# Performance work log

Measured on AMD Instinct MI355X. Metric: run time of the kernel, lower is better.

## Reference

```python
import jax, jax.numpy as jnp
import numpy as np

D_MODEL = 1024
NUM_HEADS = 16
D_K = D_MODEL // NUM_HEADS
B, S = 4, 2048


def setup_inputs() -> dict:
    key = jax.random.key(0)
    ks = jax.random.split(key, 12)
    scale = 1.0 / np.sqrt(D_MODEL)
    inp = {
        "Q": jax.random.normal(ks[0], (B, S, D_MODEL), dtype=jnp.float32),
        "K": jax.random.normal(ks[1], (B, S, D_MODEL), dtype=jnp.float32),
        "V": jax.random.normal(ks[2], (B, S, D_MODEL), dtype=jnp.float32),
        # causal mask broadcast over batch and heads; masked_fill where mask==0
        "mask": jnp.tril(jnp.ones((S, S), dtype=jnp.int32))[None, None, :, :],
        "Wq": jax.random.normal(ks[3], (D_MODEL, D_MODEL), dtype=jnp.float32) * scale,
        "bq": jnp.zeros((D_MODEL,), dtype=jnp.float32),
        "Wk": jax.random.normal(ks[4], (D_MODEL, D_MODEL), dtype=jnp.float32) * scale,
        "bk": jnp.zeros((D_MODEL,), dtype=jnp.float32),
        "Wv": jax.random.normal(ks[5], (D_MODEL, D_MODEL), dtype=jnp.float32) * scale,
        "bv": jnp.zeros((D_MODEL,), dtype=jnp.float32),
        "Wo": jax.random.normal(ks[6], (D_MODEL, D_MODEL), dtype=jnp.float32) * scale,
        "bo": jnp.zeros((D_MODEL,), dtype=jnp.float32),
    }
    return inp


def _split_heads(x):
    b, s, _ = x.shape
    return x.reshape(b, s, NUM_HEADS, D_K).transpose(0, 2, 1, 3)  # [B,H,S,Dk]


def reference(Q, K, V, mask, Wq, bq, Wk, bk, Wv, bv, Wo, bo):
    # torch nn.Linear: x @ W.T + b
    q = _split_heads(Q @ Wq.T + bq)
    k = _split_heads(K @ Wk.T + bk)
    v = _split_heads(V @ Wv.T + bv)
    scores = jnp.einsum("bhsd,bhtd->bhst", q, k) / jnp.sqrt(jnp.float32(D_K))
    scores = jnp.where(mask == 0, jnp.float32(-1e9), scores)
    probs = jax.nn.softmax(scores, axis=-1)  # dropout is identity in eval mode
    ctx = jnp.einsum("bhst,bhtd->bhsd", probs, v)
    ctx = ctx.transpose(0, 2, 1, 3).reshape(Q.shape[0], Q.shape[1], D_MODEL)
    out = ctx @ Wo.T + bo
    return out, probs
```

## Files before the change

kernel.cpp:

```cpp
#include <hip/hip_runtime.h>
#include <stdint.h>

typedef unsigned short u16;
typedef unsigned int u32;
typedef __attribute__((ext_vector_type(2))) unsigned int u32x2;
typedef __attribute__((ext_vector_type(8))) short short8;
typedef __attribute__((ext_vector_type(4))) float f32x4;
typedef __attribute__((ext_vector_type(4))) unsigned int u32x4;

#define SEQ 2048
#define DM 1024
#define NH 16
#define NBH 64
#define MR 8192

#define GLOAD16(g, l) __builtin_amdgcn_global_load_lds( \
    (const __attribute__((address_space(1))) void*)(g), \
    (__attribute__((address_space(3))) void*)(l), 16, 0, 0)

#define VMCNT(N) asm volatile("s_waitcnt vmcnt(" #N ")" ::: "memory")

__device__ __forceinline__ u16 f2bf(float f) {
  u32 u = __float_as_uint(f);
  u32 r = u + 0x7fffu + ((u >> 16) & 1u);
  return (u16)(r >> 16);
}
__device__ __forceinline__ u32 cvtpk_bf16(float lo, float hi) {
  u32 r;
  asm("v_cvt_pk_bf16_f32 %0, %1, %2" : "=v"(r) : "v"(lo), "v"(hi));
  return r;
}

__global__ __launch_bounds__(256) void cvt_all(
    const float* __restrict__ Q, const float* __restrict__ K, const float* __restrict__ V,
    const float* __restrict__ Wq, const float* __restrict__ Wk, const float* __restrict__ Wv,
    const float* __restrict__ Wo,
    u16* __restrict__ dQ, u16* __restrict__ dK, u16* __restrict__ dV,
    u16* __restrict__ dWq, u16* __restrict__ dWk, u16* __restrict__ dWv, u16* __restrict__ dWo) {
  int b = blockIdx.x;
  const float* s; u16* d; size_t off;
  if (b < 4096)       { s = Q;  d = dQ;  off = (size_t)b * 2048; }
  else if (b < 8192)  { s = K;  d = dK;  off = (size_t)(b - 4096) * 2048; }
  else if (b < 12288) { s = V;  d = dV;  off = (size_t)(b - 8192) * 2048; }
  else if (b < 12800) { s = Wq; d = dWq; off = (size_t)(b - 12288) * 2048; }
  else if (b < 13312) { s = Wk; d = dWk; off = (size_t)(b - 12800) * 2048; }
  else if (b < 13824) { s = Wv; d = dWv; off = (size_t)(b - 13312) * 2048; }
  else                { s = Wo; d = dWo; off = (size_t)(b - 13824) * 2048; }
  size_t i = off + (size_t)threadIdx.x * 8;
  float4 x = *(const float4*)(s + i);
  float4 y = *(const float4*)(s + i + 4);
  u32x4 o;
  o.x = (u32)f2bf(x.x) | ((u32)f2bf(x.y) << 16);
  o.y = (u32)f2bf(x.z) | ((u32)f2bf(x.w) << 16);
  o.z = (u32)f2bf(y.x) | ((u32)f2bf(y.y) << 16);
  o.w = (u32)f2bf(y.z) | ((u32)f2bf(y.w) << 16);
  *(u32x4*)(d + i) = o;
}

__device__ __forceinline__ void gemm_body(
    const u16* __restrict__ A, const u16* __restrict__ Bw, const float* __restrict__ bias,
    void* __restrict__ Cp, int wg, int MODE) {
  const int bn = wg & 7;
  const int bm = wg >> 3;
  __shared__ u16 As[2][128 * 64];
  __shared__ u16 Bs[2][128 * 64];
  const int tid = threadIdx.x;
  const int lane = tid & 63, wave = tid >> 6;
  const int wr = wave >> 1, wc = wave & 1;
  const int g16 = lane >> 4, l16 = lane & 15;
  f32x4 acc[4][4] = {};

  const int srow = lane >> 3;
  const int sblk = (lane & 7) ^ srow;
  const u16* Abase = A + (size_t)(bm * 128) * DM + sblk * 8;
  const u16* Bbase = Bw + (size_t)(bn * 128) * DM + sblk * 8;

  auto stage = [&](int kt) {
#pragma unroll
    for (int i = 0; i < 4; ++i) {
      const int r0 = wave * 32 + i * 8;
      GLOAD16(Abase + (size_t)(r0 + srow) * DM + kt * 64, (char*)As[kt & 1] + r0 * 128);
      GLOAD16(Bbase + (size_t)(r0 + srow) * DM + kt * 64, (char*)Bs[kt & 1] + r0 * 128);
    }
  };

  stage(0);
  for (int kt = 0; kt < 16; ++kt) {
    VMCNT(0);
    __builtin_amdgcn_s_barrier();
    if (kt + 1 < 16) stage(kt + 1);
    const char* Ab = (const char*)As[kt & 1];
    const char* Bb = (const char*)Bs[kt & 1];
#pragma unroll
    for (int ks = 0; ks < 2; ++ks) {
      short8 af[4], bfr[4];
#pragma unroll
      for (int m = 0; m < 4; ++m) {
        const int r = wr * 64 + m * 16 + l16;
        af[m] = *(const short8*)(Ab + ((r * 128 + ks * 64 + g16 * 16) ^ ((r & 7) << 4)));
      }
#pragma unroll
      for (int n = 0; n < 4; ++n) {
        const int r = wc * 64 + n * 16 + l16;
        bfr[n] = *(const short8*)(Bb + ((r * 128 + ks * 64 + g16 * 16) ^ ((r & 7) << 4)));
      }
#pragma unroll
      for (int m = 0; m < 4; ++m)
#pragma unroll
        for (int n = 0; n < 4; ++n)
          acc[m][n] = __builtin_amdgcn_mfma_f32_16x16x32_bf16(af[m], bfr[n], acc[m][n], 0, 0, 0);
    }
  }
#pragma unroll
  for (int m = 0; m < 4; ++m)
#pragma unroll
    for (int n = 0; n < 4; ++n) {
      int col = bn * 128 + wc * 64 + n * 16 + l16;
      float bs = bias[col];
      if (MODE == 2) {
        int row0 = bm * 128 + wr * 64 + m * 16 + g16 * 4;
        int bb = row0 >> 11, ss = row0 & 2047;
        int hh = col >> 6, dd = col & 63;
        u32 lo = (u32)f2bf(acc[m][n][0] + bs) | ((u32)f2bf(acc[m][n][1] + bs) << 16);
        u32 hi = (u32)f2bf(acc[m][n][2] + bs) | ((u32)f2bf(acc[m][n][3] + bs) << 16);
        *(u32x2*)((u16*)Cp + (((size_t)(bb * NH + hh) * 64 + dd) * SEQ + ss)) = (u32x2){lo, hi};
      } else {
#pragma unroll
        for (int r = 0; r < 4; ++r) {
          int row = bm * 128 + wr * 64 + m * 16 + g16 * 4 + r;
          float v = acc[m][n][r] + bs;
          if (MODE == 0) {
            int bb = row >> 11, ss = row & 2047, hh = col >> 6, dd = col & 63;
            ((u16*)Cp)[((((size_t)bb * NH + hh) * SEQ + ss) << 6) + dd] = f2bf(v);
          } else {
            ((float*)Cp)[(size_t)row * DM + col] = v;
          }
        }
      }
    }
}

__global__ __launch_bounds__(256) void gemm_qkv(
    const u16* __restrict__ Qb, const u16* __restrict__ Wqb, const float* __restrict__ bq, u16* __restrict__ qhp,
    const u16* __restrict__ Kb, const u16* __restrict__ Wkb, const float* __restrict__ bk, u16* __restrict__ khp,
    const u16* __restrict__ Vb, const u16* __restrict__ Wvb, const float* __restrict__ bv, u16* __restrict__ vtp) {
  const int bid = blockIdx.x;
  const int sel = bid >> 9;
  const int inner = bid & 511;
  const int wg = (inner & 7) * 64 + (inner >> 3);
  if (sel == 0)      gemm_body(Qb, Wqb, bq, qhp, wg, 0);
  else if (sel == 1) gemm_body(Kb, Wkb, bk, khp, wg, 0);
  else               gemm_body(Vb, Wvb, bv, vtp, wg, 2);
}

__global__ __launch_bounds__(256) void gemm_out(
    const u16* __restrict__ A, const u16* __restrict__ Bw, const float* __restrict__ bias,
    float* __restrict__ Cp) {
  const int bid = blockIdx.x;
  const int wg = (bid & 7) * 64 + (bid >> 3);
  gemm_body(A, Bw, bias, Cp, wg, 1);
}

__global__ __launch_bounds__(512, 4) void attn_fwd(
    const u16* __restrict__ qh, const u16* __restrict__ kh, const u16* __restrict__ vt,
    float* __restrict__ probs, u16* __restrict__ ctx) {
  const int bid = blockIdx.x;
  const int wg = (bid & 7) * 128 + (bid >> 3);
  const int qt = 15 - (wg & 15);
  const int bh = wg >> 4;
  const int tid = threadIdx.x;
  const int lane = tid & 63, wave = tid >> 6;
  const int g16 = lane >> 4, l16 = lane & 15;
  __shared__ __align__(16) char SLDS[65536];
  char* Ps = SLDS + 49152;

  const int qglob = qt * 128 + wave * 16 + l16;
  short8 qf0, qf1;
  {
    const u16* qp = qh + ((size_t)bh * SEQ + qglob) * 64 + g16 * 8;
    qf0 = *(const short8*)qp;
    qf1 = *(const short8*)(qp + 32);
  }
  float lrow = 0.f;
  const float SL2 = 0.125f * 1.44269504088896f;

  const int srow = wave * 8 + (lane >> 3);
  const int sblk = (lane & 7) ^ (lane >> 3);
  const u16* kS = kh + ((size_t)bh * SEQ + srow) * 64 + sblk * 8;
  const u16* vS = vt + ((size_t)bh * 64 + srow) * SEQ + sblk * 8;

  auto qk64 = [&](const char* Kb, int ss, f32x4 (&sc)[4]) {
#pragma unroll
    for (int ks = 0; ks < 2; ++ks) {
      const short8 qf = ks ? qf1 : qf0;
#pragma unroll
      for (int f = 0; f < 4; ++f) {
        const int t = ss * 64 + f * 16 + l16;
        const short8 kb = *(const short8*)(Kb + ((t * 128 + ks * 64 + g16 * 16) ^ ((t & 7) << 4)));
        sc[f] = __builtin_amdgcn_mfma_f32_16x16x32_bf16(kb, qf, sc[f], 0, 0, 0);
      }
    }
  };

  const int nkA = qt + 1;
  auto stageA = [&](int kt) {
#pragma unroll
    for (int i = 0; i < 2; ++i)
      GLOAD16(kS + ((size_t)kt * 128 + i * 64) * 64,
              SLDS + (kt & 3) * 16384 + i * 8192 + wave * 1024);
  };
  stageA(0);
  if (nkA > 1) stageA(1);
  for (int kt = 0; kt < nkA; ++kt) {
    if (kt + 2 < nkA) { stageA(kt + 2); VMCNT(4); }
    else if (kt + 1 < nkA) VMCNT(2);
    else VMCNT(0);
    __builtin_amdgcn_s_barrier();
    const char* Kb = SLDS + (kt & 3) * 16384;
    float s = 0.f;
#pragma unroll
    for (int ss = 0; ss < 2; ++ss) {
      f32x4 sc[4] = {};
      __builtin_amdgcn_s_setprio(1);
      qk64(Kb, ss, sc);
      __builtin_amdgcn_s_setprio(0);
      const bool fullt = (kt * 128 + ss * 64 + 63 <= qt * 128 + wave * 16);
      if (fullt) {
#pragma unroll
        for (int f = 0; f < 4; ++f)
#pragma unroll
          for (int r = 0; r < 4; ++r)
            s += exp2f(sc[f][r] * SL2);
      } else {
#pragma unroll
        for (int f = 0; f < 4; ++f)
#pragma unroll
          for (int r = 0; r < 4; ++r) {
            const int k = kt * 128 + ss * 64 + f * 16 + g16 * 4 + r;
            s += (k <= qglob) ? exp2f(sc[f][r] * SL2) : 0.f;
          }
      }
    }
    s += __shfl_xor(s, 16);
    s += __shfl_xor(s, 32);
    lrow += s;
  }
  const float rinv = 1.f / lrow;

  f32x4 acc[4] = {};
  const size_t prowB = ((size_t)bh * SEQ + qglob) * SEQ;
  const int prow = wave * 16 + l16;
  const int nkt = 2 * qt + 2;

  __syncthreads();
  auto stageBK = [&](int kt) {
    GLOAD16(kS + (size_t)kt * 4096, SLDS + (kt % 3) * 8192 + wave * 1024);
  };
  auto stageBV = [&](int kt) {
    GLOAD16(vS + (size_t)kt * 64, SLDS + 24576 + (kt % 3) * 8192 + wave * 1024);
  };
  stageBK(0); stageBV(0);
  for (int kt = 0; kt < nkt; ++kt) {
    if (kt + 1 < nkt) {
      stageBK(kt + 1); stageBV(kt + 1);
      if (kt == 0) VMCNT(2); else VMCNT(6);
    } else {
      if (kt == 0) VMCNT(0); else VMCNT(4);
    }
    __builtin_amdgcn_s_barrier();
    const char* Kb = SLDS + (kt % 3) * 8192;
    const char* Vb = SLDS + 24576 + (kt % 3) * 8192;
    f32x4 sc[4] = {};
    __builtin_amdgcn_s_setprio(1);
    qk64(Kb, 0, sc);
    __builtin_amdgcn_s_setprio(0);
    const bool fullt = (kt * 64 + 63 <= qt * 128 + wave * 16);
#pragma unroll
    for (int f = 0; f < 4; ++f) {
      float pv[4];
      if (fullt) {
#pragma unroll
        for (int r = 0; r < 4; ++r) pv[r] = exp2f(sc[f][r] * SL2) * rinv;
      } else {
#pragma unroll
        for (int r = 0; r < 4; ++r) {
          const int k = kt * 64 + f * 16 + g16 * 4 + r;
          pv[r] = (k <= qglob) ? exp2f(sc[f][r] * SL2) * rinv : 0.f;
        }
      }
      *(f32x4*)(probs + prowB + kt * 64 + f * 16 + g16 * 4) =
          (f32x4){pv[0], pv[1], pv[2], pv[3]};
      u32x2 pk = {cvtpk_bf16(pv[0], pv[1]), cvtpk_bf16(pv[2], pv[3])};
      *(u32x2*)(Ps + ((prow * 128 + f * 32 + g16 * 8) ^ ((prow & 7) << 4))) = pk;
    }
    __builtin_amdgcn_s_setprio(1);
#pragma unroll
    for (int ks = 0; ks < 2; ++ks) {
      const short8 pa = *(const short8*)(Ps + ((prow * 128 + ks * 64 + g16 * 16) ^ ((prow & 7) << 4)));
#pragma unroll
      for (int cf = 0; cf < 4; ++cf) {
        const int dd = cf * 16 + l16;
        const short8 vb = *(const short8*)(Vb + ((dd * 128 + ks * 64 + g16 * 16) ^ ((dd & 7) << 4)));
        acc[cf] = __builtin_amdgcn_mfma_f32_16x16x32_bf16(pa, vb, acc[cf], 0, 0, 0);
      }
    }
    __builtin_amdgcn_s_setprio(0);
  }

  {
    const size_t zrow = ((size_t)bh * SEQ + qt * 128 + wave * 16 + (lane >> 2)) * SEQ;
    const int pcol = (lane & 3) * 16;
    const f32x4 z = {0.f, 0.f, 0.f, 0.f};
    for (int c0 = nkt * 64 + pcol; c0 < SEQ; c0 += 64) {
      float* dst = probs + zrow + c0;
      *(f32x4*)(dst) = z;
      *(f32x4*)(dst + 4) = z;
      *(f32x4*)(dst + 8) = z;
      *(f32x4*)(dst + 12) = z;
    }
  }

#pragma unroll
  for (int cf = 0; cf < 4; ++cf)
#pragma unroll
    for (int r = 0; r < 4; ++r) {
      const int srw = qt * 128 + wave * 16 + g16 * 4 + r;
      const size_t o = ((size_t)(bh >> 4) * SEQ + srw) * DM + (bh & 15) * 64 + cf * 16 + l16;
      ctx[o] = f2bf(acc[cf][r]);
    }
}

extern "C" void kernel_launch(void* const* d_in, const int* in_sizes, int n_in,
                              void* d_out, int out_size, void* d_ws, size_t ws_size,
                              hipStream_t stream) {
  (void)in_sizes; (void)n_in; (void)out_size; (void)ws_size;
  const float* Q  = (const float*)d_in[0];
  const float* K  = (const float*)d_in[1];
  const float* V  = (const float*)d_in[2];
  const float* Wq = (const float*)d_in[4];
  const float* bq = (const float*)d_in[5];
  const float* Wk = (const float*)d_in[6];
  const float* bk = (const float*)d_in[7];
  const float* Wv = (const float*)d_in[8];
  const float* bv = (const float*)d_in[9];
  const float* Wo = (const float*)d_in[10];
  const float* bo = (const float*)d_in[11];

  char* ws = (char*)d_ws;
  const size_t MB = 1024 * 1024;
  u16* Qb  = (u16*)(ws + 0 * MB);
  u16* Kb  = (u16*)(ws + 16 * MB);
  u16* Vb  = (u16*)(ws + 32 * MB);
  u16* Wqb = (u16*)(ws + 48 * MB);
  u16* Wkb = (u16*)(ws + 50 * MB);
  u16* Wvb = (u16*)(ws + 52 * MB);
  u16* Wob = (u16*)(ws + 54 * MB);
  u16* qhp = (u16*)(ws + 56 * MB);
  u16* khp = (u16*)(ws + 72 * MB);
  u16* vtp = (u16*)(ws + 88 * MB);
  u16* ctx = Kb;

  float* outp = (float*)d_out;
  float* probs = outp + (size_t)MR * DM;

  cvt_all<<<14336, 256, 0, stream>>>(Q, K, V, Wq, Wk, Wv, Wo, Qb, Kb, Vb, Wqb, Wkb, Wvb, Wob);
  gemm_qkv<<<1536, 256, 0, stream>>>(Qb, Wqb, bq, qhp, Kb, Wkb, bk, khp, Vb, Wvb, bv, vtp);
  attn_fwd<<<1024, 512, 0, stream>>>(qhp, khp, vtp, probs, ctx);
  gemm_out<<<512, 256, 0, stream>>>(ctx, Wob, bo, outp);
}
```

Baseline: 472.0 us.

## Enlarge attention K/V staging tiles and switch to double-buffered barrier-first pipeline

Pass A now stages 256 keys per iteration in two 32KB buffers instead of 128 keys in a four-deep ring. Pass B moves from 64-key to 128-key K/V tiles with a new swizzled V layout, double-buffered, issuing the next prefetch after the barrier. The goal is fewer barriers and loop iterations per tile, at the cost of raising LDS from 64KB to 80KB per block. That can lower occupancy under launch_bounds(512,4), and waiting on vmcnt(0) in pass A exposes more load latency.

```diff
diff --git a/kernel.cpp b/kernel.cpp
--- a/kernel.cpp
+++ b/kernel.cpp
@@ -171,8 +171,8 @@
   const int tid = threadIdx.x;
   const int lane = tid & 63, wave = tid >> 6;
   const int g16 = lane >> 4, l16 = lane & 15;
-  __shared__ __align__(16) char SLDS[65536];
-  char* Ps = SLDS + 49152;
+  __shared__ __align__(16) char SLDS[81920];
+  char* Ps = SLDS + 65536;
 
   const int qglob = qt * 128 + wave * 16 + l16;
   short8 qf0, qf1;
@@ -187,7 +187,10 @@
   const int srow = wave * 8 + (lane >> 3);
   const int sblk = (lane & 7) ^ (lane >> 3);
   const u16* kS = kh + ((size_t)bh * SEQ + srow) * 64 + sblk * 8;
-  const u16* vS = vt + ((size_t)bh * 64 + srow) * SEQ + sblk * 8;
+  const int vrow0 = wave * 8 + (lane >> 4);
+  const u16* vS0 = vt + ((size_t)bh * 64 + vrow0) * SEQ + (((lane & 15) ^ (vrow0 & 7)) * 8);
+  const int vrow1 = vrow0 + 4;
+  const u16* vS1 = vt + ((size_t)bh * 64 + vrow1) * SEQ + (((lane & 15) ^ (vrow1 & 7)) * 8);
 
   auto qk64 = [&](const char* Kb, int ss, f32x4 (&sc)[4]) {
 #pragma unroll
@@ -202,116 +205,121 @@
     }
   };
 
-  const int nkA = qt + 1;
+  const int ntokA = (qt + 1) * 128;
+  const int n256 = (qt + 2) >> 1;
   auto stageA = [&](int kt) {
+#pragma unroll
+    for (int i = 0; i < 4; ++i)
+      GLOAD16(kS + ((size_t)kt * 256 + i * 64) * 64,
+              SLDS + (kt & 1) * 32768 + i * 8192 + wave * 1024);
+  };
+  stageA(0);
+  for (int kt = 0; kt < n256; ++kt) {
+    VMCNT(0);
+    __builtin_amdgcn_s_barrier();
+    if (kt + 1 < n256) stageA(kt + 1);
+    const char* Kb = SLDS + (kt & 1) * 32768;
+    float s = 0.f;
+#pragma unroll
+    for (int ss = 0; ss < 4; ++ss) {
+      const int t0 = kt * 256 + ss * 64;
+      if (t0 >= ntokA) break;
+      f32x4 sc[4] = {};
+      __builtin_amdgcn_s_setprio(1);
+      qk64(Kb, ss, sc);
+      __builtin_amdgcn_s_setprio(0);
+      const bool fullt = (t0 + 63 <= qt * 128 + wave * 16);
+      if (fullt) {
+#pragma unroll
+        for (int f = 0; f < 4; ++f)
+#pragma unroll
+          for (int r = 0; r < 4; ++r)
+            s += exp2f(sc[f][r] * SL2);
+      } else {
+#pragma unroll
+        for (int f = 0; f < 4; ++f)
+#pragma unroll
+          for (int r = 0; r < 4; ++r) {
+            const int k = t0 + f * 16 + g16 * 4 + r;
+            s += (k <= qglob) ? exp2f(sc[f][r] * SL2) : 0.f;
+          }
+      }
+    }
+    s += __shfl_xor(s, 16);
+    s += __shfl_xor(s, 32);
+    lrow += s;
+  }
+  const float rinv = 1.f / lrow;
+
+  f32x4 acc[4] = {};
+  const size_t prowB = ((size_t)bh * SEQ + qglob) * SEQ;
+  const int prow = wave * 16 + l16;
+  const int nkB = qt + 1;
+
+  __syncthreads();
+  auto stageBK = [&](int kt) {
 #pragma unroll
     for (int i = 0; i < 2; ++i)
       GLOAD16(kS + ((size_t)kt * 128 + i * 64) * 64,
-              SLDS + (kt & 3) * 16384 + i * 8192 + wave * 1024);
-  };
-  stageA(0);
-  if (nkA > 1) stageA(1);
-  for (int kt = 0; kt < nkA; ++kt) {
-    if (kt + 2 < nkA) { stageA(kt + 2); VMCNT(4); }
-    else if (kt + 1 < nkA) VMCNT(2);
-    else VMCNT(0);
+              SLDS + (kt & 1) * 16384 + i * 8192 + wave * 1024);
+  };
+  auto stageBV = [&](int kt) {
+    GLOAD16(vS0 + kt * 128, SLDS + 32768 + (kt & 1) * 16384 + wave * 2048);
+    GLOAD16(vS1 + kt * 128, SLDS + 32768 + (kt & 1) * 16384 + wave * 2048 + 1024);
+  };
+  stageBK(0); stageBV(0);
+  for (int kt = 0; kt < nkB; ++kt) {
+    if (kt == 0) VMCNT(0); else VMCNT(8);
     __builtin_amdgcn_s_barrier();
-    const char* Kb = SLDS + (kt & 3) * 16384;
-    float s = 0.f;
+    if (kt + 1 < nkB) { stageBK(kt + 1); stageBV(kt + 1); }
+    const char* Kb = SLDS + (kt & 1) * 16384;
+    const char* Vb = SLDS + 32768 + (kt & 1) * 16384;
 #pragma unroll
     for (int ss = 0; ss < 2; ++ss) {
       f32x4 sc[4] = {};
       __builtin_amdgcn_s_setprio(1);
       qk64(Kb, ss, sc);
       __builtin_amdgcn_s_setprio(0);
-      const bool fullt = (kt * 128 + ss * 64 + 63 <= qt * 128 + wave * 16);
-      if (fullt) {
-#pragma unroll
-        for (int f = 0; f < 4; ++f)
-#pragma unroll
-          for (int r = 0; r < 4; ++r)
-            s += exp2f(sc[f][r] * SL2);
-      } else {
-#pragma unroll
-        for (int f = 0; f < 4; ++f)
+      const int t0 = kt * 128 + ss * 64;
+      const bool fullt = (t0 + 63 <= qt * 128 + wave * 16);
+#pragma unroll
+      for (int f = 0; f < 4; ++f) {
+        float pv[4];
+        if (fullt) {
+#pragma unroll
+          for (int r = 0; r < 4; ++r) pv[r] = exp2f(sc[f][r] * SL2) * rinv;
+        } else {
 #pragma unroll
           for (int r = 0; r < 4; ++r) {
-            const int k = kt * 128 + ss * 64 + f * 16 + g16 * 4 + r;
-            s += (k <= qglob) ? exp2f(sc[f][r] * SL2) : 0.f;
+            const int k = t0 + f * 16 + g16 * 4 + r;
+            pv[r] = (k <= qglob) ? exp2f(sc[f][r] * SL2) * rinv : 0.f;
           }
-      }
-    }
-    s += __shfl_xor(s, 16);
-    s += __shfl_xor(s, 32);
-    lrow += s;
-  }
-  const float rinv = 1.f / lrow;
-
-  f32x4 acc[4] = {};
-  const size_t prowB = ((size_t)bh * SEQ + qglob) * SEQ;
-  const int prow = wave * 16 + l16;
-  const int nkt = 2 * qt + 2;
-
-  __syncthreads();
-  auto stageBK = [&](int kt) {
-    GLOAD16(kS + (size_t)kt * 4096, SLDS + (kt % 3) * 8192 + wave * 1024);
-  };
-  auto stageBV = [&](int kt) {
-    GLOAD16(vS + (size_t)kt * 64, SLDS + 24576 + (kt % 3) * 8192 + wave * 1024);
-  };
-  stageBK(0); stageBV(0);
-  for (int kt = 0; kt < nkt; ++kt) {
-    if (kt + 1 < nkt) {
-      stageBK(kt + 1); stageBV(kt + 1);
-      if (kt == 0) VMCNT(2); else VMCNT(6);
-    } else {
-      if (kt == 0) VMCNT(0); else VMCNT(4);
-    }
-    __builtin_amdgcn_s_barrier();
-    const char* Kb = SLDS + (kt % 3) * 8192;
-    const char* Vb = SLDS + 24576 + (kt % 3) * 8192;
-    f32x4 sc[4] = {};
-    __builtin_amdgcn_s_setprio(1);
-    qk64(Kb, 0, sc);
-    __builtin_amdgcn_s_setprio(0);
-    const bool fullt = (kt * 64 + 63 <= qt * 128 + wave * 16);
-#pragma unroll
-    for (int f = 0; f < 4; ++f) {
-      float pv[4];
-      if (fullt) {
-#pragma unroll
-        for (int r = 0; r < 4; ++r) pv[r] = exp2f(sc[f][r] * SL2) * rinv;
-      } else {
-#pragma unroll
-        for (int r = 0; r < 4; ++r) {
-          const int k = kt * 64 + f * 16 + g16 * 4 + r;
-          pv[r] = (k <= qglob) ? exp2f(sc[f][r] * SL2) * rinv : 0.f;
         }
-      }
-      *(f32x4*)(probs + prowB + kt * 64 + f * 16 + g16 * 4) =
-          (f32x4){pv[0], pv[1], pv[2], pv[3]};
-      u32x2 pk = {cvtpk_bf16(pv[0], pv[1]), cvtpk_bf16(pv[2], pv[3])};
-      *(u32x2*)(Ps + ((prow * 128 + f * 32 + g16 * 8) ^ ((prow & 7) << 4))) = pk;
-    }
-    __builtin_amdgcn_s_setprio(1);
-#pragma unroll
-    for (int ks = 0; ks < 2; ++ks) {
-      const short8 pa = *(const short8*)(Ps + ((prow * 128 + ks * 64 + g16 * 16) ^ ((prow & 7) << 4)));
-#pragma unroll
-      for (int cf = 0; cf < 4; ++cf) {
-        const int dd = cf * 16 + l16;
-        const short8 vb = *(const short8*)(Vb + ((dd * 128 + ks * 64 + g16 * 16) ^ ((dd & 7) << 4)));
-        acc[cf] = __builtin_amdgcn_mfma_f32_16x16x32_bf16(pa, vb, acc[cf], 0, 0, 0);
-      }
-    }
-    __builtin_amdgcn_s_setprio(0);
+        *(f32x4*)(probs + prowB + t0 + f * 16 + g16 * 4) =
+            (f32x4){pv[0], pv[1], pv[2], pv[3]};
+        u32x2 pk = {cvtpk_bf16(pv[0], pv[1]), cvtpk_bf16(pv[2], pv[3])};
+        *(u32x2*)(Ps + ((prow * 128 + f * 32 + g16 * 8) ^ ((prow & 7) << 4))) = pk;
+      }
+      __builtin_amdgcn_s_setprio(1);
+#pragma unroll
+      for (int ks = 0; ks < 2; ++ks) {
+        const short8 pa = *(const short8*)(Ps + ((prow * 128 + ks * 64 + g16 * 16) ^ ((prow & 7) << 4)));
+#pragma unroll
+        for (int cf = 0; cf < 4; ++cf) {
+          const int dd = cf * 16 + l16;
+          const short8 vb = *(const short8*)(Vb + ((dd * 256 + ss * 128 + ks * 64 + g16 * 16) ^ ((dd & 7) << 4)));
+          acc[cf] = __builtin_amdgcn_mfma_f32_16x16x32_bf16(pa, vb, acc[cf], 0, 0, 0);
+        }
+      }
+      __builtin_amdgcn_s_setprio(0);
+    }
   }
 
   {
     const size_t zrow = ((size_t)bh * SEQ + qt * 128 + wave * 16 + (lane >> 2)) * SEQ;
     const int pcol = (lane & 3) * 16;
     const f32x4 z = {0.f, 0.f, 0.f, 0.f};
-    for (int c0 = nkt * 64 + pcol; c0 < SEQ; c0 += 64) {
+    for (int c0 = nkB * 128 + pcol; c0 < SEQ; c0 += 64) {
       float* dst = probs + zrow + c0;
       *(f32x4*)(dst) = z;
       *(f32x4*)(dst + 4) = z;
```

Result: faster. 425.5 us (-9.9%).
